# Performance work log

Hardware: AMD Instinct MI355X
Metric: run time of the kernel (lower is better)

## Reference

```python
import jax, jax.numpy as jnp
import numpy as np

EMBED_DIM = 512
NUM_HEADS = 8
HEAD_DIM = EMBED_DIM // NUM_HEADS
FFN_DIM = 4 * EMBED_DIM
B, S = 4, 2048
LN_EPS = 1e-5


def _linear_params(key, fan_in, fan_out):
    kw, kb = jax.random.split(key)
    bound = 1.0 / np.sqrt(fan_in)
    W = jax.random.uniform(kw, (fan_in, fan_out), jnp.float32, -bound, bound)
    b = jax.random.uniform(kb, (fan_out,), jnp.float32, -bound, bound)
    return W, b


def setup_inputs() -> dict:
    key = jax.random.key(0)
    ks = jax.random.split(key, 10)
    query = jax.random.normal(ks[0], (B, S, EMBED_DIM), jnp.float32)
    key_t = jax.random.normal(ks[1], (B, S, EMBED_DIM), jnp.float32)
    value = jax.random.normal(ks[2], (B, S, EMBED_DIM), jnp.float32)
    Wq, bq = _linear_params(ks[3], EMBED_DIM, EMBED_DIM)
    Wk, bk = _linear_params(ks[4], EMBED_DIM, EMBED_DIM)
    Wv, bv = _linear_params(ks[5], EMBED_DIM, EMBED_DIM)
    Wo, bo = _linear_params(ks[6], EMBED_DIM, EMBED_DIM)
    W1, b1 = _linear_params(ks[7], EMBED_DIM, FFN_DIM)
    W2, b2 = _linear_params(ks[8], FFN_DIM, EMBED_DIM)
    g1 = jnp.ones((EMBED_DIM,), jnp.float32); be1 = jnp.zeros((EMBED_DIM,), jnp.float32)
    g2 = jnp.ones((EMBED_DIM,), jnp.float32); be2 = jnp.zeros((EMBED_DIM,), jnp.float32)
    return dict(query=query, key=key_t, value=value,
                Wq=Wq, bq=bq, Wk=Wk, bk=bk, Wv=Wv, bv=bv, Wo=Wo, bo=bo,
                g1=g1, be1=be1, g2=g2, be2=be2,
                W1=W1, b1=b1, W2=W2, b2=b2)


def _layernorm(x, g, b):
    mu = jnp.mean(x, axis=-1, keepdims=True)
    var = jnp.mean(jnp.square(x - mu), axis=-1, keepdims=True)
    return (x - mu) * jax.lax.rsqrt(var + LN_EPS) * g + b


def reference(query, key, value, Wq, bq, Wk, bk, Wv, bv, Wo, bo,
              g1, be1, g2, be2, W1, b1, W2, b2):
    b_, s_ = query.shape[:2]
    # projections -> [B, H, S, Dh]
    Q = (query @ Wq + bq).reshape(b_, -1, NUM_HEADS, HEAD_DIM).transpose(0, 2, 1, 3)
    K = (key @ Wk + bk).reshape(b_, -1, NUM_HEADS, HEAD_DIM).transpose(0, 2, 1, 3)
    V = (value @ Wv + bv).reshape(b_, -1, NUM_HEADS, HEAD_DIM).transpose(0, 2, 1, 3)
    scores = jnp.einsum('bhqd,bhkd->bhqk', Q, K) / jnp.sqrt(jnp.float32(HEAD_DIM))
    attn = jax.nn.softmax(scores, axis=-1)  # dropout is eval-mode identity
    ctx = jnp.einsum('bhqk,bhkd->bhqd', attn, V)
    ctx = ctx.transpose(0, 2, 1, 3).reshape(b_, -1, EMBED_DIM)
    out = ctx @ Wo + bo
    out = _layernorm(query + out, g1, be1)
    ffn = jax.nn.gelu(out @ W1 + b1, approximate=False) @ W2 + b2
    return _layernorm(out + ffn, g2, be2)
```

## Files before the change

### kernel.cpp

```cpp
#include <hip/hip_runtime.h>
#include <hip/hip_bf16.h>
#include <math.h>

#define EMBED 512
#define NHEAD 8
#define HDIM 64
#define FFN 2048
#define BB 4
#define SS 2048
#define MROWS (BB*SS)
#define NB ((size_t)MROWS * EMBED)
#define LN_EPS 1e-5f
#define QSCALE 0.180336880111f

typedef __attribute__((ext_vector_type(8))) short short8;
typedef __attribute__((ext_vector_type(4))) float floatx4;

__device__ inline float bf2f(__hip_bfloat16 x) { return __bfloat162float(x); }
__device__ inline __hip_bfloat16 f2bf(float x) { return __float2bfloat16(x); }

__device__ inline float gelu_f(float x) {
    return 0.5f * x * (1.0f + erff(x * 0.70710678118654752f));
}

__device__ inline void async_copy16(const void* g, void* l) {
    __builtin_amdgcn_global_load_lds(
        (const __attribute__((address_space(1))) void*)g,
        (__attribute__((address_space(3))) void*)l, 16, 0, 0);
}

__device__ inline int sane_f(float v) {
    return (v == v) && (fabsf(v) > 0x1p-40f) && (fabsf(v) < 0x1p40f);
}

__global__ void detect_kernel(const void* __restrict__ q, int* __restrict__ flag) {
    const float* qf = (const float*)q;
    int lane = threadIdx.x;
    float v = qf[lane * 1024 + 7];
    bool ok = sane_f(v);
    unsigned long long m = __ballot(ok);
    if (lane == 0) *flag = (__popcll(m) >= 32) ? 1 : 0;
}

__global__ __launch_bounds__(256) void prep_kernel(
    const void* __restrict__ query, const void* __restrict__ keyi, const void* __restrict__ vali,
    const void* __restrict__ Wq, const void* __restrict__ Wk, const void* __restrict__ Wv,
    const void* __restrict__ Wo, const void* __restrict__ W1, const void* __restrict__ W2,
    const void* __restrict__ bq, const void* __restrict__ bk, const void* __restrict__ bv,
    const void* __restrict__ bo, const void* __restrict__ b1, const void* __restrict__ b2,
    const void* __restrict__ g1, const void* __restrict__ be1,
    const void* __restrict__ g2, const void* __restrict__ be2,
    __hip_bfloat16* __restrict__ qkvbf,
    __hip_bfloat16* __restrict__ Wcat,
    __hip_bfloat16* __restrict__ biasb)
{
    __shared__ __hip_bfloat16 L[64][65];
    const int f32 = sane_f(((const float*)query)[7]) + sane_f(((const float*)query)[1031]) +
                    sane_f(((const float*)query)[200003]) + sane_f(((const float*)query)[1000003]) >= 3;
    const int t = threadIdx.x;
    const int blk = blockIdx.x;

    if (blk < 6144) {
        size_t pos = ((size_t)blk * 256 + t) * 8;
        int sel = (int)(pos >> 22);
        size_t off = pos & (NB - 1);
        const void* src = sel == 0 ? query : sel == 1 ? keyi : vali;
        if (f32) {
            const float* s = (const float*)src + off;
            float4 f0 = *reinterpret_cast<const float4*>(s);
            float4 f1 = *reinterpret_cast<const float4*>(s + 4);
            alignas(16) __hip_bfloat16 h[8] = {
                f2bf(f0.x), f2bf(f0.y), f2bf(f0.z), f2bf(f0.w),
                f2bf(f1.x), f2bf(f1.y), f2bf(f1.z), f2bf(f1.w)};
            *reinterpret_cast<uint4*>(qkvbf + pos) = *reinterpret_cast<const uint4*>(h);
        } else {
            *reinterpret_cast<uint4*>(qkvbf + pos) =
                *reinterpret_cast<const uint4*>((const __hip_bfloat16*)src + off);
        }
        return;
    }

    const void* src; __hip_bfloat16* dst; int R, C, r0, c0;
    if (blk < 6400) {
        int b2i = blk - 6144; src = W1; dst = Wcat + 4 * 512 * 512;
        R = 512; C = 2048; r0 = (b2i >> 5) * 64; c0 = (b2i & 31) * 64;
    } else if (blk < 6656) {
        int b3 = blk - 6400; src = W2; dst = Wcat + 4 * 512 * 512 + 512 * 2048;
        R = 2048; C = 512; r0 = (b3 >> 3) * 64; c0 = (b3 & 7) * 64;
    } else if (blk < 6912) {
        int b4 = blk - 6656; int which = b4 >> 6; int tile = b4 & 63;
        src = which == 0 ? Wq : which == 1 ? Wk : which == 2 ? Wv : Wo;
        dst = Wcat + (size_t)which * 512 * 512;
        R = 512; C = 512; r0 = (tile >> 3) * 64; c0 = (tile & 7) * 64;
    } else {
        const void* srcs[10] = {bq, bk, bv, bo, b1, b2, g1, be1, g2, be2};
        const int offs[10] = {0, 512, 1024, 1536, 2048, 4096, 4608, 5120, 5632, 6144};
        const int lens[10] = {512, 512, 512, 512, 2048, 512, 512, 512, 512, 512};
        for (int a = 0; a < 10; ++a)
            for (int i = t; i < lens[a]; i += 256)
                biasb[offs[a] + i] = f32 ? f2bf(((const float*)srcs[a])[i])
                                         : ((const __hip_bfloat16*)srcs[a])[i];
        return;
    }
    for (int c = t; c < 4096; c += 256) {
        int lr = c >> 6, lc = c & 63;
        L[lr][lc] = f32 ? f2bf(((const float*)src)[(size_t)(r0 + lr) * C + c0 + lc])
                        : ((const __hip_bfloat16*)src)[(size_t)(r0 + lr) * C + c0 + lc];
    }
    __syncthreads();
    for (int c = t; c < 4096; c += 256) {
        int lr = c >> 6, lc = c & 63;
        dst[(size_t)(c0 + lr) * R + r0 + lc] = L[lc][lr];
    }
}

template<int ACT, int BIAS>
__global__ __launch_bounds__(256) void gemm_bt_lds_kernel(
    const __hip_bfloat16* __restrict__ A,
    const __hip_bfloat16* __restrict__ Bt,
    const __hip_bfloat16* __restrict__ bias,
    __hip_bfloat16* __restrict__ C,
    int M, int N, int K, int ksplit)
{
    const int bm = blockIdx.x * 128;
    const int bn = blockIdx.y * 128;
    int kbeg = 0, kend = K;
    if (BIAS == 0) {
        kbeg = blockIdx.z * ksplit;
        kend = kbeg + ksplit;
        C += (size_t)blockIdx.z * NB;
    }
    const int t = threadIdx.x;
    const int wave = t >> 6, lane = t & 63;
    const int wm = (wave >> 1) * 64, wn = (wave & 1) * 64;
    const int quad = lane >> 4, r = lane & 15;

    __shared__ alignas(16) __hip_bfloat16 As[2][128 * 32];
    __shared__ alignas(16) __hip_bfloat16 Bs[2][128 * 32];

    floatx4 acc[4][4];
    #pragma unroll
    for (int i = 0; i < 4; ++i)
        #pragma unroll
        for (int j = 0; j < 4; ++j)
            acc[i][j] = (floatx4){0.f, 0.f, 0.f, 0.f};

    const int c0 = wave * 128;

    for (int kt = kbeg; kt < kend; kt += 64) {
        #pragma unroll
        for (int h = 0; h < 2; ++h) {
            #pragma unroll
            for (int it = 0; it < 2; ++it) {
                int c = c0 + it * 64 + lane;
                int row = c >> 2, col = (c & 3) * 8;
                async_copy16(A + (size_t)(bm + row) * K + kt + h * 32 + col,
                             As[h] + (size_t)(c0 + it * 64) * 8);
                async_copy16(Bt + (size_t)(bn + row) * K + kt + h * 32 + col,
                             Bs[h] + (size_t)(c0 + it * 64) * 8);
            }
        }
        __syncthreads();
        #pragma unroll
        for (int h = 0; h < 2; ++h) {
            short8 af[4], bfr[4];
            #pragma unroll
            for (int i = 0; i < 4; ++i)
                af[i] = *reinterpret_cast<const short8*>(&As[h][(wm + i * 16 + r) * 32 + quad * 8]);
            #pragma unroll
            for (int j = 0; j < 4; ++j)
                bfr[j] = *reinterpret_cast<const short8*>(&Bs[h][(wn + j * 16 + r) * 32 + quad * 8]);
            #pragma unroll
            for (int i = 0; i < 4; ++i)
                #pragma unroll
                for (int j = 0; j < 4; ++j)
                    acc[i][j] = __builtin_amdgcn_mfma_f32_16x16x32_bf16(af[i], bfr[j], acc[i][j], 0, 0, 0);
        }
        __syncthreads();
    }

    #pragma unroll
    for (int j = 0; j < 4; ++j) {
        const int n = bn + wn + j * 16 + r;
        float bvv = BIAS ? bf2f(bias[n]) : 0.f;
        #pragma unroll
        for (int i = 0; i < 4; ++i) {
            #pragma unroll
            for (int v = 0; v < 4; ++v) {
                int m = bm + wm + i * 16 + quad * 4 + v;
                float x = acc[i][j][v] + bvv;
                if (ACT == 1) x = gelu_f(x);
                C[(size_t)m * N + n] = f2bf(x);
            }
        }
    }
}

__global__ __launch_bounds__(256) void gemm_qkv_fused_kernel(
    const __hip_bfloat16* __restrict__ Acat,
    const __hip_bfloat16* __restrict__ Wcat,
    const __hip_bfloat16* __restrict__ biascat,
    __hip_bfloat16* __restrict__ Ocat)
{
    const int sel = blockIdx.x >> 6;
    const __hip_bfloat16* A = Acat + (size_t)sel * NB;
    const __hip_bfloat16* Bt = Wcat + (size_t)sel * 512 * 512;
    const __hip_bfloat16* bias = biascat + sel * 512;
    __hip_bfloat16* C = Ocat + (size_t)sel * NB;

    const int bm = (blockIdx.x & 63) * 128;
    const int bn = blockIdx.y * 128;
    const int t = threadIdx.x;
    const int wave = t >> 6, lane = t & 63;
    const int wm = (wave >> 1) * 64, wn = (wave & 1) * 64;
    const int quad = lane >> 4, r = lane & 15;
    const int K = EMBED, N = EMBED;

    __shared__ alignas(16) __hip_bfloat16 As[2][128 * 32];
    __shared__ alignas(16) __hip_bfloat16 Bs[2][128 * 32];

    floatx4 acc[4][4];
    #pragma unroll
    for (int i = 0; i < 4; ++i)
        #pragma unroll
        for (int j = 0; j < 4; ++j)
            acc[i][j] = (floatx4){0.f, 0.f, 0.f, 0.f};

    const int c0 = wave * 128;

    for (int kt = 0; kt < K; kt += 64) {
        #pragma unroll
        for (int h = 0; h < 2; ++h) {
            #pragma unroll
            for (int it = 0; it < 2; ++it) {
                int c = c0 + it * 64 + lane;
                int row = c >> 2, col = (c & 3) * 8;
                async_copy16(A + (size_t)(bm + row) * K + kt + h * 32 + col,
                             As[h] + (size_t)(c0 + it * 64) * 8);
                async_copy16(Bt + (size_t)(bn + row) * K + kt + h * 32 + col,
                             Bs[h] + (size_t)(c0 + it * 64) * 8);
            }
        }
        __syncthreads();
        #pragma unroll
        for (int h = 0; h < 2; ++h) {
            short8 af[4], bfr[4];
            #pragma unroll
            for (int i = 0; i < 4; ++i)
                af[i] = *reinterpret_cast<const short8*>(&As[h][(wm + i * 16 + r) * 32 + quad * 8]);
            #pragma unroll
            for (int j = 0; j < 4; ++j)
                bfr[j] = *reinterpret_cast<const short8*>(&Bs[h][(wn + j * 16 + r) * 32 + quad * 8]);
            #pragma unroll
            for (int i = 0; i < 4; ++i)
                #pragma unroll
                for (int j = 0; j < 4; ++j)
                    acc[i][j] = __builtin_amdgcn_mfma_f32_16x16x32_bf16(af[i], bfr[j], acc[i][j], 0, 0, 0);
        }
        __syncthreads();
    }

    #pragma unroll
    for (int j = 0; j < 4; ++j) {
        const int n = bn + wn + j * 16 + r;
        const float bvv = bf2f(bias[n]);
        #pragma unroll
        for (int i = 0; i < 4; ++i) {
            #pragma unroll
            for (int v = 0; v < 4; ++v) {
                int m = bm + wm + i * 16 + quad * 4 + v;
                C[(size_t)m * N + n] = f2bf(acc[i][j][v] + bvv);
            }
        }
    }
}

__global__ __launch_bounds__(256) void vtrans_kernel(
    const __hip_bfloat16* __restrict__ Vb, __hip_bfloat16* __restrict__ Vt)
{
    const int bh = blockIdx.y;
    const int b = bh >> 3, h = bh & 7;
    const int s0 = blockIdx.x * 64;
    __shared__ alignas(16) __hip_bfloat16 L[64][72];
    const int t = threadIdx.x;
    for (int c = t; c < 512; c += 256) {
        int row = c >> 3, g = c & 7;
        *reinterpret_cast<uint4*>(&L[row][g * 8]) =
            *reinterpret_cast<const uint4*>(Vb + (size_t)(b * SS + s0 + row) * EMBED + h * 64 + g * 8);
    }
    __syncthreads();
    for (int c = t; c < 512; c += 256) {
        int d = c >> 3, g = c & 7;
        alignas(16) __hip_bfloat16 tmp[8];
        #pragma unroll
        for (int j = 0; j < 8; ++j) tmp[j] = L[g * 8 + j][d];
        *reinterpret_cast<uint4*>(Vt + ((size_t)bh * 64 + d) * SS + s0 + g * 8) =
            *reinterpret_cast<const uint4*>(tmp);
    }
}

__global__ __launch_bounds__(256) void attn_mfma_kernel(
    const __hip_bfloat16* __restrict__ Qg,
    const __hip_bfloat16* __restrict__ Kg,
    const __hip_bfloat16* __restrict__ Vt,
    __hip_bfloat16* __restrict__ Apart0,
    __hip_bfloat16* __restrict__ Apart1,
    float* __restrict__ lbuf)
{
    const int bh = blockIdx.y;
    const int b = bh >> 3, h = bh & 7;
    const int q0 = blockIdx.x * 128;
    const int z = blockIdx.z;
    const int t = threadIdx.x;
    const int w = t >> 6, lane = t & 63;
    const int quad = lane >> 4, r = lane & 15;

    __shared__ alignas(16) __hip_bfloat16 Ks[2][2][64 * 32];
    __shared__ alignas(16) __hip_bfloat16 Vs[2][2][64 * 32];
    __shared__ alignas(16) __hip_bfloat16 Ps[4][32][72];

    const size_t bbase = (size_t)b * SS * EMBED;
    const size_t hoff = (size_t)h * HDIM;
    const size_t vtbase = (size_t)bh * HDIM * SS;

    short8 aq[2][2];
    #pragma unroll
    for (int s = 0; s < 2; ++s) {
        const __hip_bfloat16* qrow = Qg + bbase + (size_t)(q0 + w * 32 + s * 16 + r) * EMBED + hoff;
        short8 t0 = *reinterpret_cast<const short8*>(qrow + quad * 8);
        short8 t1 = *reinterpret_cast<const short8*>(qrow + 32 + quad * 8);
        #pragma unroll
        for (int i = 0; i < 8; ++i) {
            ((__hip_bfloat16*)&aq[s][0])[i] = f2bf(bf2f(((const __hip_bfloat16*)&t0)[i]) * QSCALE);
            ((__hip_bfloat16*)&aq[s][1])[i] = f2bf(bf2f(((const __hip_bfloat16*)&t1)[i]) * QSCALE);
        }
    }

    const short one = 0x3F80;
    const short8 bones = {one, one, one, one, one, one, one, one};

    const int tensor = w >> 1, slab = w & 1;
    const int srow = lane >> 2;
    const int scol = (((lane & 3) ^ ((srow >> 1) & 3)) * 8);
    const int cs = ((r >> 1) & 3) * 8;

    floatx4 o0[4], o1[4], l0a, l1a;
    #pragma unroll
    for (int nt = 0; nt < 4; ++nt) {
        o0[nt] = (floatx4){0.f, 0.f, 0.f, 0.f};
        o1[nt] = (floatx4){0.f, 0.f, 0.f, 0.f};
    }
    l0a = (floatx4){0.f, 0.f, 0.f, 0.f};
    l1a = (floatx4){0.f, 0.f, 0.f, 0.f};

    const int kbeg = z * (SS / 2), kend = kbeg + SS / 2;
    const __hip_bfloat16* kp[4];
    const __hip_bfloat16* vp[4];
    #pragma unroll
    for (int g = 0; g < 4; ++g) {
        int row = g * 16 + srow;
        kp[g] = Kg + bbase + (size_t)(kbeg + row) * EMBED + hoff + slab * 32 + scol;
        vp[g] = Vt + vtbase + (size_t)row * SS + kbeg + slab * 32 + scol;
    }

    if (tensor == 0) {
        #pragma unroll
        for (int g = 0; g < 4; ++g) {
            async_copy16(kp[g], &Ks[0][slab][g * 512]);
            kp[g] += 64 * EMBED;
        }
    } else {
        #pragma unroll
        for (int g = 0; g < 4; ++g) {
            async_copy16(vp[g], &Vs[0][slab][g * 512]);
            vp[g] += 64;
        }
    }
    __syncthreads();

    int cur = 0;
    for (int kt = kbeg; kt < kend; kt += 64) {
        if (kt + 64 < kend) {
            if (tensor == 0) {
                #pragma unroll
                for (int g = 0; g < 4; ++g) {
                    async_copy16(kp[g], &Ks[cur ^ 1][slab][g * 512]);
                    kp[g] += 64 * EMBED;
                }
            } else {
                #pragma unroll
                for (int g = 0; g < 4; ++g) {
                    async_copy16(vp[g], &Vs[cur ^ 1][slab][g * 512]);
                    vp[g] += 64;
                }
            }
        }

        floatx4 s0[4], s1[4];
        #pragma unroll
        for (int nt = 0; nt < 4; ++nt) {
            s0[nt] = (floatx4){0.f, 0.f, 0.f, 0.f};
            s1[nt] = (floatx4){0.f, 0.f, 0.f, 0.f};
        }
        __builtin_amdgcn_s_setprio(1);
        #pragma unroll
        for (int nt = 0; nt < 4; ++nt) {
            short8 ak0 = *reinterpret_cast<const short8*>(&Ks[cur][0][(nt * 16 + r) * 32 + (quad * 8 ^ cs)]);
            short8 ak1 = *reinterpret_cast<const short8*>(&Ks[cur][1][(nt * 16 + r) * 32 + (quad * 8 ^ cs)]);
            s0[nt] = __builtin_amdgcn_mfma_f32_16x16x32_bf16(ak0, aq[0][0], s0[nt], 0, 0, 0);
            s0[nt] = __builtin_amdgcn_mfma_f32_16x16x32_bf16(ak1, aq[0][1], s0[nt], 0, 0, 0);
            s1[nt] = __builtin_amdgcn_mfma_f32_16x16x32_bf16(ak0, aq[1][0], s1[nt], 0, 0, 0);
            s1[nt] = __builtin_amdgcn_mfma_f32_16x16x32_bf16(ak1, aq[1][1], s1[nt], 0, 0, 0);
        }
        __builtin_amdgcn_s_setprio(0);

        #pragma unroll
        for (int s = 0; s < 2; ++s) {
            floatx4* sc = s == 0 ? s0 : s1;
            #pragma unroll
            for (int nt = 0; nt < 4; ++nt) {
                float p0 = exp2f(sc[nt][0]), p1 = exp2f(sc[nt][1]);
                float p2 = exp2f(sc[nt][2]), p3 = exp2f(sc[nt][3]);
                __hip_bfloat162 pa = __float22bfloat162_rn(make_float2(p0, p1));
                __hip_bfloat162 pb = __float22bfloat162_rn(make_float2(p2, p3));
                uint2 u;
                u.x = *reinterpret_cast<unsigned*>(&pa);
                u.y = *reinterpret_cast<unsigned*>(&pb);
                *reinterpret_cast<uint2*>(&Ps[w][s * 16 + r][nt * 16 + quad * 4]) = u;
            }
        }

        short8 ap00 = *reinterpret_cast<const short8*>(&Ps[w][r][quad * 8]);
        short8 ap01 = *reinterpret_cast<const short8*>(&Ps[w][r][32 + quad * 8]);
        short8 ap10 = *reinterpret_cast<const short8*>(&Ps[w][16 + r][quad * 8]);
        short8 ap11 = *reinterpret_cast<const short8*>(&Ps[w][16 + r][32 + quad * 8]);
        __builtin_amdgcn_s_setprio(1);
        #pragma unroll
        for (int nt = 0; nt < 4; ++nt) {
            short8 bv0 = *reinterpret_cast<const short8*>(&Vs[cur][0][(nt * 16 + r) * 32 + (quad * 8 ^ cs)]);
            short8 bv1 = *reinterpret_cast<const short8*>(&Vs[cur][1][(nt * 16 + r) * 32 + (quad * 8 ^ cs)]);
            o0[nt] = __builtin_amdgcn_mfma_f32_16x16x32_bf16(ap00, bv0, o0[nt], 0, 0, 0);
            o0[nt] = __builtin_amdgcn_mfma_f32_16x16x32_bf16(ap01, bv1, o0[nt], 0, 0, 0);
            o1[nt] = __builtin_amdgcn_mfma_f32_16x16x32_bf16(ap10, bv0, o1[nt], 0, 0, 0);
            o1[nt] = __builtin_amdgcn_mfma_f32_16x16x32_bf16(ap11, bv1, o1[nt], 0, 0, 0);
        }
        l0a = __builtin_amdgcn_mfma_f32_16x16x32_bf16(ap00, bones, l0a, 0, 0, 0);
        l0a = __builtin_amdgcn_mfma_f32_16x16x32_bf16(ap01, bones, l0a, 0, 0, 0);
        l1a = __builtin_amdgcn_mfma_f32_16x16x32_bf16(ap10, bones, l1a, 0, 0, 0);
        l1a = __builtin_amdgcn_mfma_f32_16x16x32_bf16(ap11, bones, l1a, 0, 0, 0);
        __builtin_amdgcn_s_setprio(0);

        __syncthreads();
        cur ^= 1;
    }

    __hip_bfloat16* Ap = z == 0 ? Apart0 : Apart1;
    #pragma unroll
    for (int s = 0; s < 2; ++s) {
        floatx4* oa = s == 0 ? o0 : o1;
        floatx4 la = s == 0 ? l0a : l1a;
        #pragma unroll
        for (int v = 0; v < 4; ++v) {
            int q = q0 + w * 32 + s * 16 + quad * 4 + v;
            __hip_bfloat16* orow = Ap + bbase + (size_t)q * EMBED + hoff;
            #pragma unroll
            for (int nt = 0; nt < 4; ++nt)
                orow[nt * 16 + r] = f2bf(oa[nt][v]);
            if (r == 0)
                lbuf[((size_t)z * 32 + bh) * SS + q] = la[v];
        }
    }
}

__global__ __launch_bounds__(256) void attn_combine_kernel(
    const __hip_bfloat16* __restrict__ Apart0,
    const __hip_bfloat16* __restrict__ Apart1,
    const float* __restrict__ lbuf,
    __hip_bfloat16* __restrict__ ctx)
{
    const int bh = blockIdx.y;
    const int b = bh >> 3, h = bh & 7;
    const int q0 = blockIdx.x * 64;
    const int t = threadIdx.x;
    __shared__ float winv[64];

    if (t < 64) {
        float l0 = lbuf[(size_t)bh * SS + q0 + t];
        float l1 = lbuf[((size_t)32 + bh) * SS + q0 + t];
        winv[t] = 1.0f / (l0 + l1);
    }
    __syncthreads();

    const size_t base = (size_t)b * SS * EMBED + (size_t)h * HDIM;
    for (int c = t; c < 512; c += 256) {
        int q = c >> 3, d8 = (c & 7) * 8;
        size_t off = base + (size_t)(q0 + q) * EMBED + d8;
        short8 a0v = *reinterpret_cast<const short8*>(Apart0 + off);
        short8 a1v = *reinterpret_cast<const short8*>(Apart1 + off);
        float si = winv[q];
        alignas(16) __hip_bfloat16 o[8];
        #pragma unroll
        for (int j = 0; j < 8; ++j) {
            float x0 = bf2f(((const __hip_bfloat16*)&a0v)[j]);
            float x1 = bf2f(((const __hip_bfloat16*)&a1v)[j]);
            o[j] = f2bf((x0 + x1) * si);
        }
        *reinterpret_cast<uint4*>(ctx + off) = *reinterpret_cast<const uint4*>(o);
    }
}

template<int OUT32>
__global__ __launch_bounds__(256) void add_ln_split_kernel(
    const __hip_bfloat16* __restrict__ X,
    const __hip_bfloat16* __restrict__ Y0,
    const __hip_bfloat16* __restrict__ Y1,
    const __hip_bfloat16* __restrict__ bias,
    const __hip_bfloat16* __restrict__ g,
    const __hip_bfloat16* __restrict__ bt,
    void* __restrict__ out,
    const int* __restrict__ dflag)
{
    const int w = threadIdx.x >> 6, lane = threadIdx.x & 63;
    const int row = blockIdx.x * 4 + w;
    const size_t base = (size_t)row * EMBED + lane * 8;
    const int co = lane * 8;

    short8 xv  = *reinterpret_cast<const short8*>(X + base);
    short8 y0v = *reinterpret_cast<const short8*>(Y0 + base);
    short8 y1v = *reinterpret_cast<const short8*>(Y1 + base);
    short8 bv  = *reinterpret_cast<const short8*>(bias + co);

    float x[8];
    float s = 0.f;
    #pragma unroll
    for (int j = 0; j < 8; ++j) {
        x[j] = bf2f(((const __hip_bfloat16*)&xv)[j]) + bf2f(((const __hip_bfloat16*)&y0v)[j])
             + bf2f(((const __hip_bfloat16*)&y1v)[j]) + bf2f(((const __hip_bfloat16*)&bv)[j]);
        s += x[j];
    }
    #pragma unroll
    for (int off = 32; off; off >>= 1) s += __shfl_xor(s, off, 64);
    const float mu = s * (1.0f / EMBED);
    float vs = 0.f;
    #pragma unroll
    for (int j = 0; j < 8; ++j) { x[j] -= mu; vs += x[j] * x[j]; }
    #pragma unroll
    for (int off = 32; off; off >>= 1) vs += __shfl_xor(vs, off, 64);
    const float rstd = rsqrtf(vs * (1.0f / EMBED) + LN_EPS);

    short8 gv  = *reinterpret_cast<const short8*>(g + co);
    short8 btv = *reinterpret_cast<const short8*>(bt + co);
    if (OUT32 && *dflag) {
        float4 o0, o1;
        float of[8];
        #pragma unroll
        for (int j = 0; j < 8; ++j)
            of[j] = x[j] * rstd * bf2f(((const __hip_bfloat16*)&gv)[j]) + bf2f(((const __hip_bfloat16*)&btv)[j]);
        o0 = make_float4(of[0], of[1], of[2], of[3]);
        o1 = make_float4(of[4], of[5], of[6], of[7]);
        *reinterpret_cast<float4*>((float*)out + base) = o0;
        *reinterpret_cast<float4*>((float*)out + base + 4) = o1;
    } else {
        alignas(16) __hip_bfloat16 o[8];
        #pragma unroll
        for (int j = 0; j < 8; ++j)
            o[j] = f2bf(x[j] * rstd * bf2f(((const __hip_bfloat16*)&gv)[j]) + bf2f(((const __hip_bfloat16*)&btv)[j]));
        *reinterpret_cast<uint4*>((__hip_bfloat16*)out + base) = *reinterpret_cast<const uint4*>(o);
    }
}

extern "C" void kernel_launch(void* const* d_in, const int* in_sizes, int n_in,
                              void* d_out, int out_size, void* d_ws, size_t ws_size,
                              hipStream_t stream)
{
    (void)in_sizes; (void)n_in; (void)out_size; (void)ws_size;

    const void* query = d_in[0];
    const void* keyi  = d_in[1];
    const void* vali  = d_in[2];
    const void* Wq = d_in[3];  const void* bq = d_in[4];
    const void* Wk = d_in[5];  const void* bk = d_in[6];
    const void* Wv = d_in[7];  const void* bv = d_in[8];
    const void* Wo = d_in[9];  const void* bo = d_in[10];
    const void* g1 = d_in[11]; const void* be1 = d_in[12];
    const void* g2 = d_in[13]; const void* be2 = d_in[14];
    const void* W1 = d_in[15]; const void* b1 = d_in[16];
    const void* W2 = d_in[17]; const void* b2 = d_in[18];

    int* dflag = (int*)d_ws;
    __hip_bfloat16* biasb = (__hip_bfloat16*)((char*)d_ws + 64);
    __hip_bfloat16* Wcat = biasb + 8192;
    __hip_bfloat16* buf = Wcat + 4 * 512 * 512 + 2 * 512 * 2048;
    __hip_bfloat16* bqkvb = biasb;
    __hip_bfloat16* bob  = biasb + 1536;
    __hip_bfloat16* b1b  = biasb + 2048;
    __hip_bfloat16* b2b  = biasb + 4096;
    __hip_bfloat16* g1b  = biasb + 4608;
    __hip_bfloat16* be1b = biasb + 5120;
    __hip_bfloat16* g2b  = biasb + 5632;
    __hip_bfloat16* be2b = biasb + 6144;
    __hip_bfloat16* qkvbf  = buf;
    __hip_bfloat16* QKVo   = buf + 3 * NB;
    __hip_bfloat16* Qb = QKVo;
    __hip_bfloat16* Kb = QKVo + NB;
    __hip_bfloat16* Vb = QKVo + 2 * NB;
    __hip_bfloat16* Vt     = buf + 1 * NB;
    __hip_bfloat16* Apart0 = buf + 2 * NB;
    __hip_bfloat16* Apart1 = buf + 6 * NB;
    float*          lbuf   = (float*)(buf + 7 * NB);
    __hip_bfloat16* ctx    = buf + 3 * NB;
    __hip_bfloat16* Yw     = buf + 4 * NB;
    __hip_bfloat16* x1     = buf + 3 * NB;
    __hip_bfloat16* hbf    = buf + 4 * NB;
    __hip_bfloat16* Yf     = buf + 1 * NB;

    detect_kernel<<<1, 64, 0, stream>>>(query, dflag);

    prep_kernel<<<6913, 256, 0, stream>>>(
        query, keyi, vali, Wq, Wk, Wv, Wo, W1, W2,
        bq, bk, bv, bo, b1, b2, g1, be1, g2, be2,
        qkvbf, Wcat, biasb);

    gemm_qkv_fused_kernel<<<dim3(192, 4), 256, 0, stream>>>(qkvbf, Wcat, bqkvb, QKVo);

    vtrans_kernel<<<dim3(SS / 64, BB * NHEAD), 256, 0, stream>>>(Vb, Vt);

    attn_mfma_kernel<<<dim3(SS / 128, BB * NHEAD, 2), 256, 0, stream>>>(
        Qb, Kb, Vt, Apart0, Apart1, lbuf);
    attn_combine_kernel<<<dim3(SS / 64, BB * NHEAD), 256, 0, stream>>>(
        Apart0, Apart1, lbuf, ctx);

    gemm_bt_lds_kernel<0, 0><<<dim3(MROWS / 128, EMBED / 128, 2), 256, 0, stream>>>(
        ctx, Wcat + 3 * 512 * 512, nullptr, Yw, MROWS, EMBED, EMBED, EMBED / 2);
    add_ln_split_kernel<0><<<MROWS / 4, 256, 0, stream>>>(
        qkvbf, Yw, Yw + NB, bob, g1b, be1b, x1, dflag);

    gemm_bt_lds_kernel<1, 1><<<dim3(MROWS / 128, FFN / 128), 256, 0, stream>>>(
        x1, Wcat + 4 * 512 * 512, b1b, hbf, MROWS, FFN, EMBED, 0);
    gemm_bt_lds_kernel<0, 0><<<dim3(MROWS / 128, EMBED / 128, 2), 256, 0, stream>>>(
        hbf, Wcat + 4 * 512 * 512 + 512 * 2048, nullptr, Yf, MROWS, EMBED, FFN, FFN / 2);
    add_ln_split_kernel<1><<<MROWS / 4, 256, 0, stream>>>(
        x1, Yf, Yf + NB, b2b, g2b, be2b, d_out, dflag);
}
```

Before: 332.6 us.

## Double-buffer GEMM LDS tiles and drop split-K attention with its combine kernel

Both GEMM kernels now keep two LDS stages and prefetch the next K tile with async copies while MFMAs run on the current one, with one barrier per iteration instead of two. The attention kernel no longer splits the key range in two. Each block walks the full sequence and normalises its output in place, which removes the partial-output buffers, the lbuf write and the separate combine kernel launch. The costs are double the LDS per GEMM block, which may lower occupancy, and half as many attention blocks (512), so there is less parallelism on a large GPU.

```diff
diff --git a/kernel.cpp b/kernel.cpp
--- a/kernel.cpp
+++ b/kernel.cpp
@@ -135,8 +135,8 @@
     const int wm = (wave >> 1) * 64, wn = (wave & 1) * 64;
     const int quad = lane >> 4, r = lane & 15;
 
-    __shared__ alignas(16) __hip_bfloat16 As[2][128 * 32];
-    __shared__ alignas(16) __hip_bfloat16 Bs[2][128 * 32];
+    __shared__ alignas(16) __hip_bfloat16 As[2][2][128 * 32];
+    __shared__ alignas(16) __hip_bfloat16 Bs[2][2][128 * 32];
 
     floatx4 acc[4][4];
     #pragma unroll
@@ -147,7 +147,7 @@
 
     const int c0 = wave * 128;
 
-    for (int kt = kbeg; kt < kend; kt += 64) {
+    auto stage = [&](int d, int kt) {
         #pragma unroll
         for (int h = 0; h < 2; ++h) {
             #pragma unroll
@@ -155,21 +155,28 @@
                 int c = c0 + it * 64 + lane;
                 int row = c >> 2, col = (c & 3) * 8;
                 async_copy16(A + (size_t)(bm + row) * K + kt + h * 32 + col,
-                             As[h] + (size_t)(c0 + it * 64) * 8);
+                             As[d][h] + (size_t)(c0 + it * 64) * 8);
                 async_copy16(Bt + (size_t)(bn + row) * K + kt + h * 32 + col,
-                             Bs[h] + (size_t)(c0 + it * 64) * 8);
+                             Bs[d][h] + (size_t)(c0 + it * 64) * 8);
             }
         }
-        __syncthreads();
+    };
+
+    stage(0, kbeg);
+    __syncthreads();
+
+    int cur = 0;
+    for (int kt = kbeg; kt < kend; kt += 64) {
+        if (kt + 64 < kend) stage(cur ^ 1, kt + 64);
         #pragma unroll
         for (int h = 0; h < 2; ++h) {
             short8 af[4], bfr[4];
             #pragma unroll
             for (int i = 0; i < 4; ++i)
-                af[i] = *reinterpret_cast<const short8*>(&As[h][(wm + i * 16 + r) * 32 + quad * 8]);
+                af[i] = *reinterpret_cast<const short8*>(&As[cur][h][(wm + i * 16 + r) * 32 + quad * 8]);
             #pragma unroll
             for (int j = 0; j < 4; ++j)
-                bfr[j] = *reinterpret_cast<const short8*>(&Bs[h][(wn + j * 16 + r) * 32 + quad * 8]);
+                bfr[j] = *reinterpret_cast<const short8*>(&Bs[cur][h][(wn + j * 16 + r) * 32 + quad * 8]);
             #pragma unroll
             for (int i = 0; i < 4; ++i)
                 #pragma unroll
@@ -177,6 +184,7 @@
                     acc[i][j] = __builtin_amdgcn_mfma_f32_16x16x32_bf16(af[i], bfr[j], acc[i][j], 0, 0, 0);
         }
         __syncthreads();
+        cur ^= 1;
     }
 
     #pragma unroll
@@ -216,8 +224,8 @@
     const int quad = lane >> 4, r = lane & 15;
     const int K = EMBED, N = EMBED;
 
-    __shared__ alignas(16) __hip_bfloat16 As[2][128 * 32];
-    __shared__ alignas(16) __hip_bfloat16 Bs[2][128 * 32];
+    __shared__ alignas(16) __hip_bfloat16 As[2][2][128 * 32];
+    __shared__ alignas(16) __hip_bfloat16 Bs[2][2][128 * 32];
 
     floatx4 acc[4][4];
     #pragma unroll
@@ -228,7 +236,7 @@
 
     const int c0 = wave * 128;
 
-    for (int kt = 0; kt < K; kt += 64) {
+    auto stage = [&](int d, int kt) {
         #pragma unroll
         for (int h = 0; h < 2; ++h) {
             #pragma unroll
@@ -236,21 +244,28 @@
                 int c = c0 + it * 64 + lane;
                 int row = c >> 2, col = (c & 3) * 8;
                 async_copy16(A + (size_t)(bm + row) * K + kt + h * 32 + col,
-                             As[h] + (size_t)(c0 + it * 64) * 8);
+                             As[d][h] + (size_t)(c0 + it * 64) * 8);
                 async_copy16(Bt + (size_t)(bn + row) * K + kt + h * 32 + col,
-                             Bs[h] + (size_t)(c0 + it * 64) * 8);
+                             Bs[d][h] + (size_t)(c0 + it * 64) * 8);
             }
         }
-        __syncthreads();
+    };
+
+    stage(0, 0);
+    __syncthreads();
+
+    int cur = 0;
+    for (int kt = 0; kt < K; kt += 64) {
+        if (kt + 64 < K) stage(cur ^ 1, kt + 64);
         #pragma unroll
         for (int h = 0; h < 2; ++h) {
             short8 af[4], bfr[4];
             #pragma unroll
             for (int i = 0; i < 4; ++i)
-                af[i] = *reinterpret_cast<const short8*>(&As[h][(wm + i * 16 + r) * 32 + quad * 8]);
+                af[i] = *reinterpret_cast<const short8*>(&As[cur][h][(wm + i * 16 + r) * 32 + quad * 8]);
             #pragma unroll
             for (int j = 0; j < 4; ++j)
-                bfr[j] = *reinterpret_cast<const short8*>(&Bs[h][(wn + j * 16 + r) * 32 + quad * 8]);
+                bfr[j] = *reinterpret_cast<const short8*>(&Bs[cur][h][(wn + j * 16 + r) * 32 + quad * 8]);
             #pragma unroll
             for (int i = 0; i < 4; ++i)
                 #pragma unroll
@@ -258,6 +273,7 @@
                     acc[i][j] = __builtin_amdgcn_mfma_f32_16x16x32_bf16(af[i], bfr[j], acc[i][j], 0, 0, 0);
         }
         __syncthreads();
+        cur ^= 1;
     }
 
     #pragma unroll
@@ -303,14 +319,11 @@
     const __hip_bfloat16* __restrict__ Qg,
     const __hip_bfloat16* __restrict__ Kg,
     const __hip_bfloat16* __restrict__ Vt,
-    __hip_bfloat16* __restrict__ Apart0,
-    __hip_bfloat16* __restrict__ Apart1,
-    float* __restrict__ lbuf)
+    __hip_bfloat16* __restrict__ ctx)
 {
     const int bh = blockIdx.y;
     const int b = bh >> 3, h = bh & 7;
     const int q0 = blockIdx.x * 128;
-    const int z = blockIdx.z;
     const int t = threadIdx.x;
     const int w = t >> 6, lane = t & 63;
     const int quad = lane >> 4, r = lane & 15;
@@ -353,14 +366,13 @@
     l0a = (floatx4){0.f, 0.f, 0.f, 0.f};
     l1a = (floatx4){0.f, 0.f, 0.f, 0.f};
 
-    const int kbeg = z * (SS / 2), kend = kbeg + SS / 2;
     const __hip_bfloat16* kp[4];
     const __hip_bfloat16* vp[4];
     #pragma unroll
     for (int g = 0; g < 4; ++g) {
         int row = g * 16 + srow;
-        kp[g] = Kg + bbase + (size_t)(kbeg + row) * EMBED + hoff + slab * 32 + scol;
-        vp[g] = Vt + vtbase + (size_t)row * SS + kbeg + slab * 32 + scol;
+        kp[g] = Kg + bbase + (size_t)row * EMBED + hoff + slab * 32 + scol;
+        vp[g] = Vt + vtbase + (size_t)row * SS + slab * 32 + scol;
     }
 
     if (tensor == 0) {
@@ -379,8 +391,8 @@
     __syncthreads();
 
     int cur = 0;
-    for (int kt = kbeg; kt < kend; kt += 64) {
-        if (kt + 64 < kend) {
+    for (int kt = 0; kt < SS; kt += 64) {
+        if (kt + 64 < SS) {
             if (tensor == 0) {
                 #pragma unroll
                 for (int g = 0; g < 4; ++g) {
@@ -454,7 +466,6 @@
         cur ^= 1;
     }
 
-    __hip_bfloat16* Ap = z == 0 ? Apart0 : Apart1;
     #pragma unroll
     for (int s = 0; s < 2; ++s) {
         floatx4* oa = s == 0 ? o0 : o1;
@@ -462,50 +473,12 @@
         #pragma unroll
         for (int v = 0; v < 4; ++v) {
             int q = q0 + w * 32 + s * 16 + quad * 4 + v;
-            __hip_bfloat16* orow = Ap + bbase + (size_t)q * EMBED + hoff;
+            float inv = 1.0f / la[v];
+            __hip_bfloat16* orow = ctx + bbase + (size_t)q * EMBED + hoff;
             #pragma unroll
             for (int nt = 0; nt < 4; ++nt)
-                orow[nt * 16 + r] = f2bf(oa[nt][v]);
-            if (r == 0)
-                lbuf[((size_t)z * 32 + bh) * SS + q] = la[v];
-        }
-    }
-}
-
-__global__ __launch_bounds__(256) void attn_combine_kernel(
-    const __hip_bfloat16* __restrict__ Apart0,
-    const __hip_bfloat16* __restrict__ Apart1,
-    const float* __restrict__ lbuf,
-    __hip_bfloat16* __restrict__ ctx)
-{
-    const int bh = blockIdx.y;
-    const int b = bh >> 3, h = bh & 7;
-    const int q0 = blockIdx.x * 64;
-    const int t = threadIdx.x;
-    __shared__ float winv[64];
-
-    if (t < 64) {
-        float l0 = lbuf[(size_t)bh * SS + q0 + t];
-        float l1 = lbuf[((size_t)32 + bh) * SS + q0 + t];
-        winv[t] = 1.0f / (l0 + l1);
-    }
-    __syncthreads();
-
-    const size_t base = (size_t)b * SS * EMBED + (size_t)h * HDIM;
-    for (int c = t; c < 512; c += 256) {
-        int q = c >> 3, d8 = (c & 7) * 8;
-        size_t off = base + (size_t)(q0 + q) * EMBED + d8;
-        short8 a0v = *reinterpret_cast<const short8*>(Apart0 + off);
-        short8 a1v = *reinterpret_cast<const short8*>(Apart1 + off);
-        float si = winv[q];
-        alignas(16) __hip_bfloat16 o[8];
-        #pragma unroll
-        for (int j = 0; j < 8; ++j) {
-            float x0 = bf2f(((const __hip_bfloat16*)&a0v)[j]);
-            float x1 = bf2f(((const __hip_bfloat16*)&a1v)[j]);
-            o[j] = f2bf((x0 + x1) * si);
-        }
-        *reinterpret_cast<uint4*>(ctx + off) = *reinterpret_cast<const uint4*>(o);
+                orow[nt * 16 + r] = f2bf(oa[nt][v] * inv);
+        }
     }
 }
 
@@ -605,10 +578,7 @@
     __hip_bfloat16* Kb = QKVo + NB;
     __hip_bfloat16* Vb = QKVo + 2 * NB;
     __hip_bfloat16* Vt     = buf + 1 * NB;
-    __hip_bfloat16* Apart0 = buf + 2 * NB;
-    __hip_bfloat16* Apart1 = buf + 6 * NB;
-    float*          lbuf   = (float*)(buf + 7 * NB);
-    __hip_bfloat16* ctx    = buf + 3 * NB;
+    __hip_bfloat16* ctx    = buf + 2 * NB;
     __hip_bfloat16* Yw     = buf + 4 * NB;
     __hip_bfloat16* x1     = buf + 3 * NB;
     __hip_bfloat16* hbf    = buf + 4 * NB;
@@ -625,10 +595,8 @@
 
     vtrans_kernel<<<dim3(SS / 64, BB * NHEAD), 256, 0, stream>>>(Vb, Vt);
 
-    attn_mfma_kernel<<<dim3(SS / 128, BB * NHEAD, 2), 256, 0, stream>>>(
-        Qb, Kb, Vt, Apart0, Apart1, lbuf);
-    attn_combine_kernel<<<dim3(SS / 64, BB * NHEAD), 256, 0, stream>>>(
-        Apart0, Apart1, lbuf, ctx);
+    attn_mfma_kernel<<<dim3(SS / 128, BB * NHEAD), 256, 0, stream>>>(
+        Qb, Kb, Vt, ctx);
 
     gemm_bt_lds_kernel<0, 0><<<dim3(MROWS / 128, EMBED / 128, 2), 256, 0, stream>>>(
         ctx, Wcat + 3 * 512 * 512, nullptr, Yw, MROWS, EMBED, EMBED, EMBED / 2);
```

Result: no change. 330.3 us (-0.7%).
